# Performance work log

Measured on AMD Instinct MI355X. Metric: run time of the kernel, lower is better.

Reference implementation:

```python
import jax, jax.numpy as jnp
import numpy as np

N_NODES = 400
HID = 96
DEC = 64
FEAT_STATIC = 8
FEAT = FEAT_STATIC + N_NODES  # 408
EPS = 1e-8


def prelu(x, a):
    # single-parameter PReLU (torch default num_parameters=1)
    return jnp.where(x >= 0, x, a * x)


def setup_inputs() -> dict:
    key = jax.random.key(0)
    ks = jax.random.split(key, 16)
    B = 16
    E = N_NODES * (N_NODES - 1) // 2  # 79800

    x = jax.random.normal(ks[0], (B, E), dtype=jnp.float32)
    node_features = jax.random.normal(ks[1], (B, N_NODES, FEAT_STATIC), dtype=jnp.float32)
    sc_matrix = jax.random.uniform(ks[2], (B, N_NODES, N_NODES), dtype=jnp.float32)

    # normalization buffers (computed from train split in torch; random stand-ins)
    static_mean = jax.random.normal(ks[3], (1, 1, FEAT_STATIC), dtype=jnp.float32) * 0.1
    static_std = jnp.ones((1, 1, FEAT_STATIC), dtype=jnp.float32)

    def lin(k, fin, fout):
        kw, kb = jax.random.split(k)
        lim = 1.0 / np.sqrt(fin)
        W = jax.random.uniform(kw, (fin, fout), minval=-lim, maxval=lim, dtype=jnp.float32)
        b = jax.random.uniform(kb, (fout,), minval=-lim, maxval=lim, dtype=jnp.float32)
        return W, b

    W_e1, b_e1 = lin(ks[4], FEAT, HID)
    W_e2, b_e2 = lin(ks[5], HID, HID)
    W_d1, b_d1 = lin(ks[6], 3 * HID, DEC)  # symmetric decoder: 3 * node_embed_dim
    W_d2, b_d2 = lin(ks[7], DEC, DEC)
    W_d3, b_d3 = lin(ks[8], DEC, 1)

    a25 = jnp.float32(0.25)

    ei_np, ej_np = np.triu_indices(N_NODES, k=1)
    ei = jnp.asarray(ei_np, dtype=jnp.int32)
    ej = jnp.asarray(ej_np, dtype=jnp.int32)

    return {
        "x": x, "node_features": node_features, "sc_matrix": sc_matrix,
        "static_mean": static_mean, "static_std": static_std,
        "W_e1": W_e1, "b_e1": b_e1, "a_e1": a25,
        "W_e2": W_e2, "b_e2": b_e2, "a_e2": a25,
        "W_d1": W_d1, "b_d1": b_d1, "a_d1": a25,
        "W_d2": W_d2, "b_d2": b_d2, "a_d2": a25,
        "W_d3": W_d3, "b_d3": b_d3,
        "ei": ei, "ej": ej,
    }


def reference(x, node_features, sc_matrix, static_mean, static_std,
              W_e1, b_e1, a_e1, W_e2, b_e2, a_e2,
              W_d1, b_d1, a_d1, W_d2, b_d2, a_d2, W_d3, b_d3, ei, ej):
    # x (SC upper triangle) is only used for batch size in the torch module.
    # static anatomical block: z-score with train stats
    s = (node_features - static_mean) / (static_std + EPS)  # [B,N,8]
    # sc_row block, 'brain_scale': divide by per-matrix mean
    m = sc_matrix / jnp.maximum(
        jnp.mean(sc_matrix, axis=(-2, -1), keepdims=True), EPS)  # [B,N,N]
    feats = jnp.concatenate([s, m], axis=-1)  # [B,N,408]

    # shared node encoder (dropout inactive at eval)
    h = prelu(feats @ W_e1 + b_e1, a_e1)
    h = prelu(h @ W_e2 + b_e2, a_e2)  # [B,N,96]

    # per-edge gather over upper-triangle indices
    h_i = h[:, ei, :]  # [B,E,96]
    h_j = h[:, ej, :]
    # symmetric edge features
    edge_feat = jnp.concatenate(
        [h_i + h_j, jnp.abs(h_i - h_j), h_i * h_j], axis=-1)  # [B,E,288]

    z = prelu(edge_feat @ W_d1 + b_d1, a_d1)
    z = prelu(z @ W_d2 + b_d2, a_d2)
    out = (z @ W_d3 + b_d3)[..., 0]  # [B,E]
    return out
```

## Files before the change

kernel.cpp:

```cpp
#include <hip/hip_runtime.h>

#define NN 400
#define HID 96
#define EDGES 79800
#define BATCH 16
#define ROWS (BATCH*EDGES)
#define NT 13
#define NPAIRS 91

typedef _Float16 f16;
typedef f16 f16x2 __attribute__((ext_vector_type(2)));
typedef f16 f16x8 __attribute__((ext_vector_type(8)));
typedef __fp16 fp16x2 __attribute__((ext_vector_type(2)));
typedef float f32x16 __attribute__((ext_vector_type(16)));
typedef unsigned int u32;
typedef unsigned long long u64;

union H8 { f16x8 h; u32 u[4]; f16x2 p[4]; fp16x2 q[4]; u64 d[2]; };
union C2 { f16x2 h; fp16x2 q; u32 u; };

__device__ inline f16x2 pkrtz(float a, float b) {
  C2 c; c.q = __builtin_amdgcn_cvt_pkrtz(a, b); return c.h;
}
__device__ inline u32 pkrtz_u(float a, float b) {
  C2 c; c.q = __builtin_amdgcn_cvt_pkrtz(a, b); return c.u;
}
__device__ inline float fdot2a(f16x2 a, f16x2 b, float c) {
#if __has_builtin(__builtin_amdgcn_fdot2)
  C2 ca, cb; ca.h = a; cb.h = b;
  return __builtin_amdgcn_fdot2(ca.q, cb.q, c, false);
#else
  return c + (float)a.x*(float)b.x + (float)a.y*(float)b.y;
#endif
}

__device__ inline f16x8 habs8(f16x8 x) {
  H8 t; t.h = x;
  t.u[0] &= 0x7fff7fffu; t.u[1] &= 0x7fff7fffu;
  t.u[2] &= 0x7fff7fffu; t.u[3] &= 0x7fff7fffu;
  return t.h;
}

__device__ inline f16x8 pack8(float a0,float a1,float a2,float a3,
                              float a4,float a5,float a6,float a7){
  H8 u;
  u.p[0] = pkrtz(a0,a1);
  u.p[1] = pkrtz(a2,a3);
  u.p[2] = pkrtz(a4,a5);
  u.p[3] = pkrtz(a6,a7);
  return u.h;
}

__global__ void prep_mean_kernel(const float* __restrict__ We1, const float* __restrict__ We2,
                                 const float* __restrict__ W1, const float* __restrict__ W2,
                                 const float* __restrict__ sc,
                                 u32* __restrict__ wq, float* __restrict__ mpart) {
  if (blockIdx.x >= 140) {
    int p = blockIdx.x - 140;
    int b = p >> 4, part = p & 15;
    const float4* src = (const float4*)(sc + (size_t)b*160000) + part*2500;
    float s = 0.f;
    for (int i = threadIdx.x; i < 2500; i += 256) {
      float4 v = src[i];
      s += (v.x + v.y) + (v.z + v.w);
    }
    __shared__ float red[256];
    red[threadIdx.x] = s; __syncthreads();
    for (int off = 128; off > 0; off >>= 1) {
      if (threadIdx.x < off) red[threadIdx.x] += red[threadIdx.x + off];
      __syncthreads();
    }
    if (threadIdx.x == 0) mpart[p] = red[0];
    return;
  }
  int D = blockIdx.x*256 + threadIdx.x;
  float v0, v1;
  if (D < 9216) {
    int frag = D >> 8;  int t = frag >> 1, q = frag & 1;
    int rem = D & 255;  int lane = rem >> 2, dj = rem & 3;
    int c = lane & 31, h2 = lane >> 5;
    int k = 16*t + 8*h2 + 2*dj;
    int d = 32*q + c;
    v0 = W1[k*64 + d]; v1 = W1[(k+1)*64 + d];
  } else if (D < 11264) {
    int Dl = D - 9216;
    int frag = Dl >> 8; int t2 = frag >> 1, q = frag & 1;
    int rem = Dl & 255; int lane = rem >> 2, dj = rem & 3;
    int c = lane & 31, h2 = lane >> 5;
    int p = 8*t2 + 4*h2 + dj;
    int d = 32*q + c;
    v0 = W2[p*64 + d]; v1 = W2[(p+32)*64 + d];
  } else if (D < 31232) {
    int Dl = D - 11264;
    int frag = Dl >> 8; int t = frag/3, ct = frag - 3*t;
    int rem = Dl & 255; int lane = rem >> 2, dj = rem & 3;
    int c = lane & 31, h2 = lane >> 5;
    int k0 = 16*t + 8*h2 + 2*dj, k1 = k0 + 1;
    int d = 32*ct + c;
    v0 = (k0 < 400) ? We1[(8+k0)*96 + d] : (k0 < 408 ? We1[(k0-400)*96 + d] : 0.f);
    v1 = (k1 < 400) ? We1[(8+k1)*96 + d] : (k1 < 408 ? We1[(k1-400)*96 + d] : 0.f);
  } else {
    int Dl = D - 31232;
    int frag = Dl >> 8; int t = frag/3, ct = frag - 3*t;
    int rem = Dl & 255; int lane = rem >> 2, dj = rem & 3;
    int c = lane & 31, h2 = lane >> 5;
    int k = 16*t + 8*h2 + 2*dj;
    int d = 32*ct + c;
    v0 = We2[k*96 + d]; v1 = We2[(k+1)*96 + d];
  }
  wq[D] = pkrtz_u(v0, v1);
}

__global__ __launch_bounds__(256) void enc_kernel(
    const float* __restrict__ sc, const float* __restrict__ nf,
    const float* __restrict__ smean, const float* __restrict__ sstd,
    const float* __restrict__ be1, const float* __restrict__ ae1,
    const float* __restrict__ be2, const float* __restrict__ ae2,
    const float* __restrict__ mpart, const u32* __restrict__ wq,
    f16* __restrict__ hout) {
  __shared__ u32 lds[12288 + 1664];
  const int tid = threadIdx.x;
  const int wid = tid >> 6, lane = tid & 63;
  const int c = lane & 31, h2 = lane >> 5;
  const int r0 = blockIdx.x * 32;
  {
    int row = tid >> 3, seg = tid & 7;
    int r = r0 + row;
    int b = r / 400;
    float ms = 0.f;
    const float4* mp4 = (const float4*)(mpart + 16*b);
#pragma unroll
    for (int k = 0; k < 4; ++k) { float4 v = mp4[k]; ms += (v.x+v.y)+(v.z+v.w); }
    float rm = 1.f / fmaxf(ms*(1.f/160000.f), 1e-8f);
    const float4* src = (const float4*)(sc + (size_t)r*400);
#pragma unroll
    for (int i = 0; i < 13; ++i) {
      int col4 = seg + 8*i;
      if (col4 < 100) {
        float4 v = src[col4];
        u32 lo = pkrtz_u(v.x*rm, v.y*rm);
        u32 hi = pkrtz_u(v.z*rm, v.w*rm);
        *(u64*)(lds + row*210 + col4*2) = (u64)lo | ((u64)hi << 32);
      }
    }
  }
  __syncthreads();
  int tb = (wid==0) ? 0 : (wid==1) ? 7 : (wid==2) ? 14 : 20;
  int te = (wid==0) ? 7 : (wid==1) ? 14 : (wid==2) ? 20 : 26;
  f32x16 acc[3] = {};
  const u32* wb1 = wq + 11264;
  for (int t = tb; t < te; ++t) {
    f16x8 af;
    if (t < 25) {
      H8 av;
      const u32* ap = lds + c*210 + 8*t + 4*h2;
      av.d[0] = *(const u64*)ap;
      av.d[1] = *(const u64*)(ap + 2);
      af = av.h;
    } else {
      af = (f16x8){};
      if (h2 == 0) {
        int r = r0 + c;
        float q0[8];
#pragma unroll
        for (int j = 0; j < 8; ++j)
          q0[j] = (nf[r*8 + j] - smean[j]) / (sstd[j] + 1e-8f);
        af = pack8(q0[0],q0[1],q0[2],q0[3],q0[4],q0[5],q0[6],q0[7]);
      }
    }
#pragma unroll
    for (int ct = 0; ct < 3; ++ct) {
      f16x8 bf = *(const f16x8*)(wb1 + ((t*3+ct)*64 + lane)*4);
      acc[ct] = __builtin_amdgcn_mfma_f32_32x32x16_f16(af, bf, acc[ct], 0,0,0);
    }
  }
  __syncthreads();
#pragma unroll
  for (int ct = 0; ct < 3; ++ct) {
    union { f32x16 v; float4 f[4]; } u; u.v = acc[ct];
#pragma unroll
    for (int i4 = 0; i4 < 4; ++i4)
      *(float4*)(lds + (((wid*3+ct)*4 + i4)*64 + lane)*4) = u.f[i4];
  }
  __syncthreads();
  f16* zb16 = (f16*)(lds + 12288);
  const float a1 = *ae1;
  if (wid < 3) {
    float bv = be1[32*wid + c];
    f32x16 s;
#pragma unroll
    for (int i = 0; i < 16; ++i) s[i] = bv;
#pragma unroll
    for (int w2 = 0; w2 < 4; ++w2) {
#pragma unroll
      for (int i4 = 0; i4 < 4; ++i4) {
        float4 f = *(const float4*)(lds + (((w2*3+wid)*4 + i4)*64 + lane)*4);
        s[4*i4+0] += f.x; s[4*i4+1] += f.y; s[4*i4+2] += f.z; s[4*i4+3] += f.w;
      }
    }
#pragma unroll
    for (int r = 0; r < 16; ++r) {
      float v = s[r]; v = fmaxf(v, a1*v);
      int row = (r & 3) + 8*(r >> 2) + 4*h2;
      zb16[row*104 + 32*wid + c] = (f16)v;
    }
  }
  __syncthreads();
  if (wid < 3) {
    const float a2 = *ae2;
    float bv = be2[32*wid + c];
    f32x16 acc2;
#pragma unroll
    for (int i = 0; i < 16; ++i) acc2[i] = bv;
    const u32* wb2 = wq + 31232;
#pragma unroll
    for (int t = 0; t < 6; ++t) {
      f16x8 af = *(const f16x8*)(zb16 + c*104 + 16*t + 8*h2);
      f16x8 bf = *(const f16x8*)(wb2 + ((t*3+wid)*64 + lane)*4);
      acc2 = __builtin_amdgcn_mfma_f32_32x32x16_f16(af, bf, acc2, 0,0,0);
    }
#pragma unroll
    for (int rr = 0; rr < 16; ++rr) {
      int row = (rr & 3) + 8*(rr >> 2) + 4*h2;
      float v = acc2[rr]; v = fmaxf(v, a2*v);
      hout[(r0 + row)*96 + 32*wid + c] = (f16)v;
    }
  }
}

__global__ __launch_bounds__(256, 2) void decoder_kernel(
    const f16* __restrict__ hbuf, const u32* __restrict__ wq,
    const float* __restrict__ b1, const float* __restrict__ b2,
    const float* __restrict__ ad1, const float* __restrict__ ad2,
    const float* __restrict__ W3, const float* __restrict__ b3p,
    float* __restrict__ out) {
  __shared__ alignas(16) u32 smem[15360];
  const int tid = threadIdx.x;
  int p = blockIdx.x;
  int b = p / NPAIRS, pr = p - b*NPAIRS;
  int I = 0;
  while (pr >= NT - I) { pr -= NT - I; ++I; }
  const int J = I + pr;
  {
    for (int idx = tid; idx < 384; idx += 256) {
      int rr = idx / 12, ch = idx - rr*12;
      int nb = I*32 + rr;
      nb = nb < NN ? nb : NN-1;
      *(float4*)(smem + rr*48 + ch*4) =
          *(const float4*)(hbuf + (size_t)(b*NN + nb)*HID + ch*8);
    }
  }
  {
    float4* dst = (float4*)(smem + 1536);
    const float4* srcw = (const float4*)wq;
#pragma unroll
    for (int k = 0; k < 9; ++k) dst[tid + 256*k] = srcw[tid + 256*k];
  }

  const int lane = tid & 63;
  const int wid  = tid >> 6;
  const int c = lane & 31, h2 = lane >> 5;
  f16x8 hjr[6];
  {
    int nbJ = J*32 + c; nbJ = nbJ < NN ? nbJ : NN-1;
    const f16* hjrow = hbuf + (size_t)(b*NN + nbJ)*HID + 8*h2;
#pragma unroll
    for (int t = 0; t < 6; ++t) hjr[t] = *(const f16x8*)(hjrow + 16*t);
  }
  __syncthreads();

  const f16* hIlds = (const f16*)smem;
  const f16* wfr = (const f16*)(smem + 1536);
  u32* zb = smem + 10752 + wid*1152;
  f16x8 w2f[4][2];
#pragma unroll
  for (int t2 = 0; t2 < 4; ++t2) {
    w2f[t2][0] = *(const f16x8*)(wq + 9216 + ((t2*2+0)*64 + lane)*4);
    w2f[t2][1] = *(const f16x8*)(wq + 9216 + ((t2*2+1)*64 + lane)*4);
  }
  const float b1x = b1[c], b1y = b1[c+32];
  const float b2x = b2[c], b2y = b2[c+32];
  const float a1 = *ad1, a2 = *ad2, b3 = *b3p;
  const f16x2 a1v = pkrtz(a1, a1);
  const f16x2 a2v = pkrtz(a2, a2);
  const f16x2 w3p = pkrtz(W3[c], W3[c+32]);
  const f16x2 ones2 = pkrtz(1.f, 1.f);
  const int gj = J*32 + c;
  const int bofs = b*EDGES;

  for (int it = 0; it < 4; ++it) {
    const int i0 = it*8 + wid*2;
    const f16* hi0p = hIlds + (i0+0)*HID + 8*h2;
    const f16* hi1p = hIlds + (i0+1)*HID + 8*h2;
    f32x16 acc[2][2];
#pragma unroll
    for (int r = 0; r < 16; ++r) {
      acc[0][0][r] = b1x; acc[0][1][r] = b1y;
      acc[1][0][r] = b1x; acc[1][1][r] = b1y;
    }
#pragma unroll
    for (int t = 0; t < 6; ++t) {
      f16x8 bs0 = *(const f16x8*)(wfr + (((t   )*2+0)*64 + lane)*8);
      f16x8 bs1 = *(const f16x8*)(wfr + (((t   )*2+1)*64 + lane)*8);
      f16x8 bd0 = *(const f16x8*)(wfr + (((t+ 6)*2+0)*64 + lane)*8);
      f16x8 bd1 = *(const f16x8*)(wfr + (((t+ 6)*2+1)*64 + lane)*8);
      f16x8 bp0 = *(const f16x8*)(wfr + (((t+12)*2+0)*64 + lane)*8);
      f16x8 bp1 = *(const f16x8*)(wfr + (((t+12)*2+1)*64 + lane)*8);
      f16x8 hj = hjr[t];
#pragma unroll
      for (int m = 0; m < 2; ++m) {
        f16x8 hi = *(const f16x8*)((m ? hi1p : hi0p) + 16*t);
        f16x8 su = hi + hj;
        f16x8 di = habs8(hi - hj);
        f16x8 prd = hi * hj;
        acc[m][0] = __builtin_amdgcn_mfma_f32_32x32x16_f16(su, bs0, acc[m][0], 0,0,0);
        acc[m][1] = __builtin_amdgcn_mfma_f32_32x32x16_f16(su, bs1, acc[m][1], 0,0,0);
        acc[m][0] = __builtin_amdgcn_mfma_f32_32x32x16_f16(di, bd0, acc[m][0], 0,0,0);
        acc[m][1] = __builtin_amdgcn_mfma_f32_32x32x16_f16(di, bd1, acc[m][1], 0,0,0);
        acc[m][0] = __builtin_amdgcn_mfma_f32_32x32x16_f16(prd, bp0, acc[m][0], 0,0,0);
        acc[m][1] = __builtin_amdgcn_mfma_f32_32x32x16_f16(prd, bp1, acc[m][1], 0,0,0);
      }
    }
#pragma unroll
    for (int m = 0; m < 2; ++m) {
#pragma unroll
      for (int r = 0; r < 16; ++r) {
        f16x2 pz = pkrtz(acc[m][0][r], acc[m][1][r]);
        pz = __builtin_elementwise_max(pz, pz * a1v);
        C2 cv; cv.h = pz;
        int row = (r & 3) + 8*(r >> 2) + 4*h2;
        zb[row*36 + c] = cv.u;
      }
      f16x8 za[4];
#pragma unroll
      for (int t2 = 0; t2 < 4; ++t2)
        za[t2] = *(const f16x8*)((const f16*)zb + (c*36 + 8*t2 + 4*h2)*2);
      f32x16 zacc[2];
#pragma unroll
      for (int r = 0; r < 16; ++r) { zacc[0][r] = b2x; zacc[1][r] = b2y; }
#pragma unroll
      for (int t2 = 0; t2 < 4; ++t2) {
        zacc[0] = __builtin_amdgcn_mfma_f32_32x32x16_f16(za[t2], w2f[t2][0], zacc[0], 0,0,0);
        zacc[1] = __builtin_amdgcn_mfma_f32_32x32x16_f16(za[t2], w2f[t2][1], zacc[1], 0,0,0);
      }
#pragma unroll
      for (int r = 0; r < 16; ++r) {
        f16x2 pz = pkrtz(zacc[0][r], zacc[1][r]);
        pz = __builtin_elementwise_max(pz, pz * a2v);
        pz = pz * w3p;
        C2 cv; cv.h = pz;
        int row = (r & 3) + 8*(r >> 2) + 4*h2;
        zb[row*36 + c] = cv.u;
      }
      float ssum = 0.f;
#pragma unroll
      for (int g = 0; g < 4; ++g) {
        H8 v; v.h = *(const f16x8*)((const f16*)zb + (c*36 + 16*h2 + 4*g)*2);
#pragma unroll
        for (int dw = 0; dw < 4; ++dw)
          ssum = fdot2a(v.p[dw], ones2, ssum);
      }
      ssum += __shfl_xor(ssum, 32);
      int gi = I*32 + i0 + m;
      bool valid = (gi < gj) && (gj < NN);
      if (h2 == 0 && valid) {
        int eo = bofs + gi*(799 - gi)/2 + (gj - gi - 1);
        out[eo] = ssum + b3;
      }
    }
  }
}

extern "C" void kernel_launch(void* const* d_in, const int* in_sizes, int n_in,
                              void* d_out, int out_size, void* d_ws, size_t ws_size,
                              hipStream_t stream) {
  const float* nf  = (const float*)d_in[1];
  const float* sc  = (const float*)d_in[2];
  const float* sm  = (const float*)d_in[3];
  const float* ss  = (const float*)d_in[4];
  const float* We1 = (const float*)d_in[5];
  const float* be1 = (const float*)d_in[6];
  const float* ae1 = (const float*)d_in[7];
  const float* We2 = (const float*)d_in[8];
  const float* be2 = (const float*)d_in[9];
  const float* ae2 = (const float*)d_in[10];
  const float* W1  = (const float*)d_in[11];
  const float* b1  = (const float*)d_in[12];
  const float* a1  = (const float*)d_in[13];
  const float* W2  = (const float*)d_in[14];
  const float* b2  = (const float*)d_in[15];
  const float* a2  = (const float*)d_in[16];
  const float* W3  = (const float*)d_in[17];
  const float* b3  = (const float*)d_in[18];
  float* out = (float*)d_out;

  char* ws = (char*)d_ws;
  float* mpart = (float*)ws;
  f16*   hbuf = (f16*)(ws + 1024);
  u32*   wq   = (u32*)(ws + 1024 + 1228800);

  prep_mean_kernel<<<396, 256, 0, stream>>>(We1, We2, W1, W2, sc, wq, mpart);
  enc_kernel<<<200, 256, 0, stream>>>(sc, nf, sm, ss, be1, ae1, be2, ae2,
                                      mpart, wq, hbuf);
  decoder_kernel<<<BATCH*NPAIRS, 256, 0, stream>>>(hbuf, wq, b1, b2, a1, a2,
                                                   W3, b3, out);
}
```

Baseline: 185.6 us.

## Fuse prep, encoder and decoder into one persistent kernel with grid barriers

Replaces three kernel launches with a single persistent kernel of 512 blocks that runs weight packing and the mean reduction, the node encoder and then the edge decoder. Between phases it synchronises through atomic-counter grid barriers that are reset by a memset each call. The decoder now loops over pair tasks with a block stride and loads the decoder weights into shared memory once per block. The aim is to remove launch gaps and tail idling between stages. In exchange it adds barrier spin cost and an extra memset, and it relies on all 512 blocks being resident at once to avoid deadlock.

Measured after the change: 239.2 us. 1.29x slower.

```diff
diff --git a/kernel.cpp b/kernel.cpp
--- a/kernel.cpp
+++ b/kernel.cpp
@@ -7,6 +7,7 @@
 #define ROWS (BATCH*EDGES)
 #define NT 13
 #define NPAIRS 91
+#define NBLK 512
 
 typedef _Float16 f16;
 typedef f16 f16x2 __attribute__((ext_vector_type(2)));
@@ -51,321 +52,332 @@
   return u.h;
 }
 
-__global__ void prep_mean_kernel(const float* __restrict__ We1, const float* __restrict__ We2,
-                                 const float* __restrict__ W1, const float* __restrict__ W2,
-                                 const float* __restrict__ sc,
-                                 u32* __restrict__ wq, float* __restrict__ mpart) {
-  if (blockIdx.x >= 140) {
-    int p = blockIdx.x - 140;
+__device__ inline void grid_barrier(u32* ctr) {
+  __syncthreads();
+  if (threadIdx.x == 0) {
+    __builtin_amdgcn_fence(__ATOMIC_RELEASE, "agent");
+    atomicAdd(ctr, 1u);
+    while (__hip_atomic_load(ctr, __ATOMIC_RELAXED, __HIP_MEMORY_SCOPE_AGENT) < (u32)NBLK)
+      __builtin_amdgcn_s_sleep(2);
+    __builtin_amdgcn_fence(__ATOMIC_ACQUIRE, "agent");
+  }
+  __syncthreads();
+}
+
+__global__ __launch_bounds__(256, 2) void mega_kernel(
+    const float* __restrict__ nf, const float* __restrict__ sc,
+    const float* __restrict__ sm, const float* __restrict__ ss,
+    const float* __restrict__ We1, const float* __restrict__ be1, const float* __restrict__ ae1,
+    const float* __restrict__ We2, const float* __restrict__ be2, const float* __restrict__ ae2,
+    const float* __restrict__ W1, const float* __restrict__ b1, const float* __restrict__ ad1,
+    const float* __restrict__ W2, const float* __restrict__ b2, const float* __restrict__ ad2,
+    const float* __restrict__ W3, const float* __restrict__ b3p,
+    float* __restrict__ out, u32* __restrict__ ctr, float* __restrict__ mpart,
+    f16* __restrict__ hbuf, u32* __restrict__ wq)
+{
+  __shared__ alignas(16) u32 smem[15360];
+  const int tid = threadIdx.x;
+  const int bid = blockIdx.x;
+
+  if (bid < 140) {
+    int D = bid*256 + tid;
+    float v0, v1;
+    if (D < 9216) {
+      int frag = D >> 8;  int t = frag >> 1, q = frag & 1;
+      int rem = D & 255;  int lane = rem >> 2, dj = rem & 3;
+      int c = lane & 31, h2 = lane >> 5;
+      int k = 16*t + 8*h2 + 2*dj;
+      int d = 32*q + c;
+      v0 = W1[k*64 + d]; v1 = W1[(k+1)*64 + d];
+    } else if (D < 11264) {
+      int Dl = D - 9216;
+      int frag = Dl >> 8; int t2 = frag >> 1, q = frag & 1;
+      int rem = Dl & 255; int lane = rem >> 2, dj = rem & 3;
+      int c = lane & 31, h2 = lane >> 5;
+      int p = 8*t2 + 4*h2 + dj;
+      int d = 32*q + c;
+      v0 = W2[p*64 + d]; v1 = W2[(p+32)*64 + d];
+    } else if (D < 31232) {
+      int Dl = D - 11264;
+      int frag = Dl >> 8; int t = frag/3, ct = frag - 3*t;
+      int rem = Dl & 255; int lane = rem >> 2, dj = rem & 3;
+      int c = lane & 31, h2 = lane >> 5;
+      int k0 = 16*t + 8*h2 + 2*dj, k1 = k0 + 1;
+      int d = 32*ct + c;
+      v0 = (k0 < 400) ? We1[(8+k0)*96 + d] : (k0 < 408 ? We1[(k0-400)*96 + d] : 0.f);
+      v1 = (k1 < 400) ? We1[(8+k1)*96 + d] : (k1 < 408 ? We1[(k1-400)*96 + d] : 0.f);
+    } else {
+      int Dl = D - 31232;
+      int frag = Dl >> 8; int t = frag/3, ct = frag - 3*t;
+      int rem = Dl & 255; int lane = rem >> 2, dj = rem & 3;
+      int c = lane & 31, h2 = lane >> 5;
+      int k = 16*t + 8*h2 + 2*dj;
+      int d = 32*ct + c;
+      v0 = We2[k*96 + d]; v1 = We2[(k+1)*96 + d];
+    }
+    wq[D] = pkrtz_u(v0, v1);
+  } else if (bid < 396) {
+    int p = bid - 140;
     int b = p >> 4, part = p & 15;
     const float4* src = (const float4*)(sc + (size_t)b*160000) + part*2500;
     float s = 0.f;
-    for (int i = threadIdx.x; i < 2500; i += 256) {
+    for (int i = tid; i < 2500; i += 256) {
       float4 v = src[i];
       s += (v.x + v.y) + (v.z + v.w);
     }
-    __shared__ float red[256];
-    red[threadIdx.x] = s; __syncthreads();
+    float* red = (float*)smem;
+    red[tid] = s; __syncthreads();
     for (int off = 128; off > 0; off >>= 1) {
-      if (threadIdx.x < off) red[threadIdx.x] += red[threadIdx.x + off];
+      if (tid < off) red[tid] += red[tid + off];
       __syncthreads();
     }
-    if (threadIdx.x == 0) mpart[p] = red[0];
-    return;
+    if (tid == 0) mpart[p] = red[0];
   }
-  int D = blockIdx.x*256 + threadIdx.x;
-  float v0, v1;
-  if (D < 9216) {
-    int frag = D >> 8;  int t = frag >> 1, q = frag & 1;
-    int rem = D & 255;  int lane = rem >> 2, dj = rem & 3;
-    int c = lane & 31, h2 = lane >> 5;
-    int k = 16*t + 8*h2 + 2*dj;
-    int d = 32*q + c;
-    v0 = W1[k*64 + d]; v1 = W1[(k+1)*64 + d];
-  } else if (D < 11264) {
-    int Dl = D - 9216;
-    int frag = Dl >> 8; int t2 = frag >> 1, q = frag & 1;
-    int rem = Dl & 255; int lane = rem >> 2, dj = rem & 3;
-    int c = lane & 31, h2 = lane >> 5;
-    int p = 8*t2 + 4*h2 + dj;
-    int d = 32*q + c;
-    v0 = W2[p*64 + d]; v1 = W2[(p+32)*64 + d];
-  } else if (D < 31232) {
-    int Dl = D - 11264;
-    int frag = Dl >> 8; int t = frag/3, ct = frag - 3*t;
-    int rem = Dl & 255; int lane = rem >> 2, dj = rem & 3;
-    int c = lane & 31, h2 = lane >> 5;
-    int k0 = 16*t + 8*h2 + 2*dj, k1 = k0 + 1;
-    int d = 32*ct + c;
-    v0 = (k0 < 400) ? We1[(8+k0)*96 + d] : (k0 < 408 ? We1[(k0-400)*96 + d] : 0.f);
-    v1 = (k1 < 400) ? We1[(8+k1)*96 + d] : (k1 < 408 ? We1[(k1-400)*96 + d] : 0.f);
-  } else {
-    int Dl = D - 31232;
-    int frag = Dl >> 8; int t = frag/3, ct = frag - 3*t;
-    int rem = Dl & 255; int lane = rem >> 2, dj = rem & 3;
-    int c = lane & 31, h2 = lane >> 5;
-    int k = 16*t + 8*h2 + 2*dj;
-    int d = 32*ct + c;
-    v0 = We2[k*96 + d]; v1 = We2[(k+1)*96 + d];
+  grid_barrier(ctr);
+
+  if (bid < 200) {
+    u32* lds = smem;
+    const int wid = tid >> 6, lane = tid & 63;
+    const int c = lane & 31, h2 = lane >> 5;
+    const int r0 = bid * 32;
+    {
+      int row = tid >> 3, seg = tid & 7;
+      int r = r0 + row;
+      int b = r / 400;
+      float ms = 0.f;
+      const float4* mp4 = (const float4*)(mpart + 16*b);
+#pragma unroll
+      for (int k = 0; k < 4; ++k) { float4 v = mp4[k]; ms += (v.x+v.y)+(v.z+v.w); }
+      float rm = 1.f / fmaxf(ms*(1.f/160000.f), 1e-8f);
+      const float4* src = (const float4*)(sc + (size_t)r*400);
+#pragma unroll
+      for (int i = 0; i < 13; ++i) {
+        int col4 = seg + 8*i;
+        if (col4 < 100) {
+          float4 v = src[col4];
+          u32 lo = pkrtz_u(v.x*rm, v.y*rm);
+          u32 hi = pkrtz_u(v.z*rm, v.w*rm);
+          *(u64*)(lds + row*210 + col4*2) = (u64)lo | ((u64)hi << 32);
+        }
+      }
+    }
+    __syncthreads();
+    int tb = (wid==0) ? 0 : (wid==1) ? 7 : (wid==2) ? 14 : 20;
+    int te = (wid==0) ? 7 : (wid==1) ? 14 : (wid==2) ? 20 : 26;
+    f32x16 acc[3] = {};
+    const u32* wb1 = wq + 11264;
+    for (int t = tb; t < te; ++t) {
+      f16x8 af;
+      if (t < 25) {
+        H8 av;
+        const u32* ap = lds + c*210 + 8*t + 4*h2;
+        av.d[0] = *(const u64*)ap;
+        av.d[1] = *(const u64*)(ap + 2);
+        af = av.h;
+      } else {
+        af = (f16x8){};
+        if (h2 == 0) {
+          int r = r0 + c;
+          float q0[8];
+#pragma unroll
+          for (int j = 0; j < 8; ++j)
+            q0[j] = (nf[r*8 + j] - sm[j]) / (ss[j] + 1e-8f);
+          af = pack8(q0[0],q0[1],q0[2],q0[3],q0[4],q0[5],q0[6],q0[7]);
+        }
+      }
+#pragma unroll
+      for (int ct = 0; ct < 3; ++ct) {
+        f16x8 bf = *(const f16x8*)(wb1 + ((t*3+ct)*64 + lane)*4);
+        acc[ct] = __builtin_amdgcn_mfma_f32_32x32x16_f16(af, bf, acc[ct], 0,0,0);
+      }
+    }
+    __syncthreads();
+#pragma unroll
+    for (int ct = 0; ct < 3; ++ct) {
+      union { f32x16 v; float4 f[4]; } u; u.v = acc[ct];
+#pragma unroll
+      for (int i4 = 0; i4 < 4; ++i4)
+        *(float4*)(lds + (((wid*3+ct)*4 + i4)*64 + lane)*4) = u.f[i4];
+    }
+    __syncthreads();
+    f16* zb16 = (f16*)(lds + 12288);
+    const float a1 = *ae1;
+    if (wid < 3) {
+      float bv = be1[32*wid + c];
+      f32x16 s;
+#pragma unroll
+      for (int i = 0; i < 16; ++i) s[i] = bv;
+#pragma unroll
+      for (int w2 = 0; w2 < 4; ++w2) {
+#pragma unroll
+        for (int i4 = 0; i4 < 4; ++i4) {
+          float4 f = *(const float4*)(lds + (((w2*3+wid)*4 + i4)*64 + lane)*4);
+          s[4*i4+0] += f.x; s[4*i4+1] += f.y; s[4*i4+2] += f.z; s[4*i4+3] += f.w;
+        }
+      }
+#pragma unroll
+      for (int r = 0; r < 16; ++r) {
+        float v = s[r]; v = fmaxf(v, a1*v);
+        int row = (r & 3) + 8*(r >> 2) + 4*h2;
+        zb16[row*104 + 32*wid + c] = (f16)v;
+      }
+    }
+    __syncthreads();
+    if (wid < 3) {
+      const float a2 = *ae2;
+      float bv = be2[32*wid + c];
+      f32x16 acc2;
+#pragma unroll
+      for (int i = 0; i < 16; ++i) acc2[i] = bv;
+      const u32* wb2 = wq + 31232;
+#pragma unroll
+      for (int t = 0; t < 6; ++t) {
+        f16x8 af = *(const f16x8*)(zb16 + c*104 + 16*t + 8*h2);
+        f16x8 bf = *(const f16x8*)(wb2 + ((t*3+wid)*64 + lane)*4);
+        acc2 = __builtin_amdgcn_mfma_f32_32x32x16_f16(af, bf, acc2, 0,0,0);
+      }
+#pragma unroll
+      for (int rr = 0; rr < 16; ++rr) {
+        int row = (rr & 3) + 8*(rr >> 2) + 4*h2;
+        float v = acc2[rr]; v = fmaxf(v, a2*v);
+        hbuf[(r0 + row)*96 + 32*wid + c] = (f16)v;
+      }
+    }
   }
-  wq[D] = pkrtz_u(v0, v1);
-}
-
-__global__ __launch_bounds__(256) void enc_kernel(
-    const float* __restrict__ sc, const float* __restrict__ nf,
-    const float* __restrict__ smean, const float* __restrict__ sstd,
-    const float* __restrict__ be1, const float* __restrict__ ae1,
-    const float* __restrict__ be2, const float* __restrict__ ae2,
-    const float* __restrict__ mpart, const u32* __restrict__ wq,
-    f16* __restrict__ hout) {
-  __shared__ u32 lds[12288 + 1664];
-  const int tid = threadIdx.x;
-  const int wid = tid >> 6, lane = tid & 63;
-  const int c = lane & 31, h2 = lane >> 5;
-  const int r0 = blockIdx.x * 32;
+  grid_barrier(ctr + 32);
+
   {
-    int row = tid >> 3, seg = tid & 7;
-    int r = r0 + row;
-    int b = r / 400;
-    float ms = 0.f;
-    const float4* mp4 = (const float4*)(mpart + 16*b);
-#pragma unroll
-    for (int k = 0; k < 4; ++k) { float4 v = mp4[k]; ms += (v.x+v.y)+(v.z+v.w); }
-    float rm = 1.f / fmaxf(ms*(1.f/160000.f), 1e-8f);
-    const float4* src = (const float4*)(sc + (size_t)r*400);
-#pragma unroll
-    for (int i = 0; i < 13; ++i) {
-      int col4 = seg + 8*i;
-      if (col4 < 100) {
-        float4 v = src[col4];
-        u32 lo = pkrtz_u(v.x*rm, v.y*rm);
-        u32 hi = pkrtz_u(v.z*rm, v.w*rm);
-        *(u64*)(lds + row*210 + col4*2) = (u64)lo | ((u64)hi << 32);
-      }
-    }
-  }
-  __syncthreads();
-  int tb = (wid==0) ? 0 : (wid==1) ? 7 : (wid==2) ? 14 : 20;
-  int te = (wid==0) ? 7 : (wid==1) ? 14 : (wid==2) ? 20 : 26;
-  f32x16 acc[3] = {};
-  const u32* wb1 = wq + 11264;
-  for (int t = tb; t < te; ++t) {
-    f16x8 af;
-    if (t < 25) {
-      H8 av;
-      const u32* ap = lds + c*210 + 8*t + 4*h2;
-      av.d[0] = *(const u64*)ap;
-      av.d[1] = *(const u64*)(ap + 2);
-      af = av.h;
-    } else {
-      af = (f16x8){};
-      if (h2 == 0) {
-        int r = r0 + c;
-        float q0[8];
-#pragma unroll
-        for (int j = 0; j < 8; ++j)
-          q0[j] = (nf[r*8 + j] - smean[j]) / (sstd[j] + 1e-8f);
-        af = pack8(q0[0],q0[1],q0[2],q0[3],q0[4],q0[5],q0[6],q0[7]);
-      }
-    }
-#pragma unroll
-    for (int ct = 0; ct < 3; ++ct) {
-      f16x8 bf = *(const f16x8*)(wb1 + ((t*3+ct)*64 + lane)*4);
-      acc[ct] = __builtin_amdgcn_mfma_f32_32x32x16_f16(af, bf, acc[ct], 0,0,0);
-    }
-  }
-  __syncthreads();
-#pragma unroll
-  for (int ct = 0; ct < 3; ++ct) {
-    union { f32x16 v; float4 f[4]; } u; u.v = acc[ct];
-#pragma unroll
-    for (int i4 = 0; i4 < 4; ++i4)
-      *(float4*)(lds + (((wid*3+ct)*4 + i4)*64 + lane)*4) = u.f[i4];
-  }
-  __syncthreads();
-  f16* zb16 = (f16*)(lds + 12288);
-  const float a1 = *ae1;
-  if (wid < 3) {
-    float bv = be1[32*wid + c];
-    f32x16 s;
-#pragma unroll
-    for (int i = 0; i < 16; ++i) s[i] = bv;
-#pragma unroll
-    for (int w2 = 0; w2 < 4; ++w2) {
-#pragma unroll
-      for (int i4 = 0; i4 < 4; ++i4) {
-        float4 f = *(const float4*)(lds + (((w2*3+wid)*4 + i4)*64 + lane)*4);
-        s[4*i4+0] += f.x; s[4*i4+1] += f.y; s[4*i4+2] += f.z; s[4*i4+3] += f.w;
-      }
-    }
-#pragma unroll
-    for (int r = 0; r < 16; ++r) {
-      float v = s[r]; v = fmaxf(v, a1*v);
-      int row = (r & 3) + 8*(r >> 2) + 4*h2;
-      zb16[row*104 + 32*wid + c] = (f16)v;
-    }
-  }
-  __syncthreads();
-  if (wid < 3) {
-    const float a2 = *ae2;
-    float bv = be2[32*wid + c];
-    f32x16 acc2;
-#pragma unroll
-    for (int i = 0; i < 16; ++i) acc2[i] = bv;
-    const u32* wb2 = wq + 31232;
-#pragma unroll
-    for (int t = 0; t < 6; ++t) {
-      f16x8 af = *(const f16x8*)(zb16 + c*104 + 16*t + 8*h2);
-      f16x8 bf = *(const f16x8*)(wb2 + ((t*3+wid)*64 + lane)*4);
-      acc2 = __builtin_amdgcn_mfma_f32_32x32x16_f16(af, bf, acc2, 0,0,0);
-    }
-#pragma unroll
-    for (int rr = 0; rr < 16; ++rr) {
-      int row = (rr & 3) + 8*(rr >> 2) + 4*h2;
-      float v = acc2[rr]; v = fmaxf(v, a2*v);
-      hout[(r0 + row)*96 + 32*wid + c] = (f16)v;
-    }
-  }
-}
-
-__global__ __launch_bounds__(256, 2) void decoder_kernel(
-    const f16* __restrict__ hbuf, const u32* __restrict__ wq,
-    const float* __restrict__ b1, const float* __restrict__ b2,
-    const float* __restrict__ ad1, const float* __restrict__ ad2,
-    const float* __restrict__ W3, const float* __restrict__ b3p,
-    float* __restrict__ out) {
-  __shared__ alignas(16) u32 smem[15360];
-  const int tid = threadIdx.x;
-  int p = blockIdx.x;
-  int b = p / NPAIRS, pr = p - b*NPAIRS;
-  int I = 0;
-  while (pr >= NT - I) { pr -= NT - I; ++I; }
-  const int J = I + pr;
-  {
-    for (int idx = tid; idx < 384; idx += 256) {
-      int rr = idx / 12, ch = idx - rr*12;
-      int nb = I*32 + rr;
-      nb = nb < NN ? nb : NN-1;
-      *(float4*)(smem + rr*48 + ch*4) =
-          *(const float4*)(hbuf + (size_t)(b*NN + nb)*HID + ch*8);
-    }
-  }
-  {
-    float4* dst = (float4*)(smem + 1536);
-    const float4* srcw = (const float4*)wq;
-#pragma unroll
-    for (int k = 0; k < 9; ++k) dst[tid + 256*k] = srcw[tid + 256*k];
-  }
-
-  const int lane = tid & 63;
-  const int wid  = tid >> 6;
-  const int c = lane & 31, h2 = lane >> 5;
-  f16x8 hjr[6];
-  {
-    int nbJ = J*32 + c; nbJ = nbJ < NN ? nbJ : NN-1;
-    const f16* hjrow = hbuf + (size_t)(b*NN + nbJ)*HID + 8*h2;
-#pragma unroll
-    for (int t = 0; t < 6; ++t) hjr[t] = *(const f16x8*)(hjrow + 16*t);
-  }
-  __syncthreads();
-
-  const f16* hIlds = (const f16*)smem;
-  const f16* wfr = (const f16*)(smem + 1536);
-  u32* zb = smem + 10752 + wid*1152;
-  f16x8 w2f[4][2];
-#pragma unroll
-  for (int t2 = 0; t2 < 4; ++t2) {
-    w2f[t2][0] = *(const f16x8*)(wq + 9216 + ((t2*2+0)*64 + lane)*4);
-    w2f[t2][1] = *(const f16x8*)(wq + 9216 + ((t2*2+1)*64 + lane)*4);
-  }
-  const float b1x = b1[c], b1y = b1[c+32];
-  const float b2x = b2[c], b2y = b2[c+32];
-  const float a1 = *ad1, a2 = *ad2, b3 = *b3p;
-  const f16x2 a1v = pkrtz(a1, a1);
-  const f16x2 a2v = pkrtz(a2, a2);
-  const f16x2 w3p = pkrtz(W3[c], W3[c+32]);
-  const f16x2 ones2 = pkrtz(1.f, 1.f);
-  const int gj = J*32 + c;
-  const int bofs = b*EDGES;
-
-  for (int it = 0; it < 4; ++it) {
-    const int i0 = it*8 + wid*2;
-    const f16* hi0p = hIlds + (i0+0)*HID + 8*h2;
-    const f16* hi1p = hIlds + (i0+1)*HID + 8*h2;
-    f32x16 acc[2][2];
-#pragma unroll
-    for (int r = 0; r < 16; ++r) {
-      acc[0][0][r] = b1x; acc[0][1][r] = b1y;
-      acc[1][0][r] = b1x; acc[1][1][r] = b1y;
-    }
-#pragma unroll
-    for (int t = 0; t < 6; ++t) {
-      f16x8 bs0 = *(const f16x8*)(wfr + (((t   )*2+0)*64 + lane)*8);
-      f16x8 bs1 = *(const f16x8*)(wfr + (((t   )*2+1)*64 + lane)*8);
-      f16x8 bd0 = *(const f16x8*)(wfr + (((t+ 6)*2+0)*64 + lane)*8);
-      f16x8 bd1 = *(const f16x8*)(wfr + (((t+ 6)*2+1)*64 + lane)*8);
-      f16x8 bp0 = *(const f16x8*)(wfr + (((t+12)*2+0)*64 + lane)*8);
-      f16x8 bp1 = *(const f16x8*)(wfr + (((t+12)*2+1)*64 + lane)*8);
-      f16x8 hj = hjr[t];
-#pragma unroll
-      for (int m = 0; m < 2; ++m) {
-        f16x8 hi = *(const f16x8*)((m ? hi1p : hi0p) + 16*t);
-        f16x8 su = hi + hj;
-        f16x8 di = habs8(hi - hj);
-        f16x8 prd = hi * hj;
-        acc[m][0] = __builtin_amdgcn_mfma_f32_32x32x16_f16(su, bs0, acc[m][0], 0,0,0);
-        acc[m][1] = __builtin_amdgcn_mfma_f32_32x32x16_f16(su, bs1, acc[m][1], 0,0,0);
-        acc[m][0] = __builtin_amdgcn_mfma_f32_32x32x16_f16(di, bd0, acc[m][0], 0,0,0);
-        acc[m][1] = __builtin_amdgcn_mfma_f32_32x32x16_f16(di, bd1, acc[m][1], 0,0,0);
-        acc[m][0] = __builtin_amdgcn_mfma_f32_32x32x16_f16(prd, bp0, acc[m][0], 0,0,0);
-        acc[m][1] = __builtin_amdgcn_mfma_f32_32x32x16_f16(prd, bp1, acc[m][1], 0,0,0);
-      }
-    }
-#pragma unroll
-    for (int m = 0; m < 2; ++m) {
-#pragma unroll
-      for (int r = 0; r < 16; ++r) {
-        f16x2 pz = pkrtz(acc[m][0][r], acc[m][1][r]);
-        pz = __builtin_elementwise_max(pz, pz * a1v);
-        C2 cv; cv.h = pz;
-        int row = (r & 3) + 8*(r >> 2) + 4*h2;
-        zb[row*36 + c] = cv.u;
-      }
-      f16x8 za[4];
-#pragma unroll
-      for (int t2 = 0; t2 < 4; ++t2)
-        za[t2] = *(const f16x8*)((const f16*)zb + (c*36 + 8*t2 + 4*h2)*2);
-      f32x16 zacc[2];
-#pragma unroll
-      for (int r = 0; r < 16; ++r) { zacc[0][r] = b2x; zacc[1][r] = b2y; }
-#pragma unroll
-      for (int t2 = 0; t2 < 4; ++t2) {
-        zacc[0] = __builtin_amdgcn_mfma_f32_32x32x16_f16(za[t2], w2f[t2][0], zacc[0], 0,0,0);
-        zacc[1] = __builtin_amdgcn_mfma_f32_32x32x16_f16(za[t2], w2f[t2][1], zacc[1], 0,0,0);
-      }
-#pragma unroll
-      for (int r = 0; r < 16; ++r) {
-        f16x2 pz = pkrtz(zacc[0][r], zacc[1][r]);
-        pz = __builtin_elementwise_max(pz, pz * a2v);
-        pz = pz * w3p;
-        C2 cv; cv.h = pz;
-        int row = (r & 3) + 8*(r >> 2) + 4*h2;
-        zb[row*36 + c] = cv.u;
-      }
-      float ssum = 0.f;
-#pragma unroll
-      for (int g = 0; g < 4; ++g) {
-        H8 v; v.h = *(const f16x8*)((const f16*)zb + (c*36 + 16*h2 + 4*g)*2);
-#pragma unroll
-        for (int dw = 0; dw < 4; ++dw)
-          ssum = fdot2a(v.p[dw], ones2, ssum);
-      }
-      ssum += __shfl_xor(ssum, 32);
-      int gi = I*32 + i0 + m;
-      bool valid = (gi < gj) && (gj < NN);
-      if (h2 == 0 && valid) {
-        int eo = bofs + gi*(799 - gi)/2 + (gj - gi - 1);
-        out[eo] = ssum + b3;
+    const int lane = tid & 63;
+    const int wid  = tid >> 6;
+    const int c = lane & 31, h2 = lane >> 5;
+    __syncthreads();
+    {
+      float4* dst = (float4*)(smem + 1536);
+      const float4* srcw = (const float4*)wq;
+#pragma unroll
+      for (int k = 0; k < 9; ++k) dst[tid + 256*k] = srcw[tid + 256*k];
+    }
+    const f16* hIlds = (const f16*)smem;
+    const f16* wfr = (const f16*)(smem + 1536);
+    u32* zb = smem + 10752 + wid*1152;
+    f16x8 w2f[4][2];
+#pragma unroll
+    for (int t2 = 0; t2 < 4; ++t2) {
+      w2f[t2][0] = *(const f16x8*)(wq + 9216 + ((t2*2+0)*64 + lane)*4);
+      w2f[t2][1] = *(const f16x8*)(wq + 9216 + ((t2*2+1)*64 + lane)*4);
+    }
+    const float b1x = b1[c], b1y = b1[c+32];
+    const float b2x = b2[c], b2y = b2[c+32];
+    const float a1 = *ad1, a2 = *ad2, b3 = *b3p;
+    const f16x2 a1v = pkrtz(a1, a1);
+    const f16x2 a2v = pkrtz(a2, a2);
+    const f16x2 w3p = pkrtz(W3[c], W3[c+32]);
+    const f16x2 ones2 = pkrtz(1.f, 1.f);
+
+    for (int task = bid; task < BATCH*NPAIRS; task += NBLK) {
+      int b = task / NPAIRS, pr = task - b*NPAIRS;
+      int I = 0;
+      while (pr >= NT - I) { pr -= NT - I; ++I; }
+      const int J = I + pr;
+      __syncthreads();
+      for (int idx = tid; idx < 384; idx += 256) {
+        int rr = idx / 12, ch = idx - rr*12;
+        int nb = I*32 + rr;
+        nb = nb < NN ? nb : NN-1;
+        *(float4*)(smem + rr*48 + ch*4) =
+            *(const float4*)(hbuf + (size_t)(b*NN + nb)*HID + ch*8);
+      }
+      f16x8 hjr[6];
+      {
+        int nbJ = J*32 + c; nbJ = nbJ < NN ? nbJ : NN-1;
+        const f16* hjrow = hbuf + (size_t)(b*NN + nbJ)*HID + 8*h2;
+#pragma unroll
+        for (int t = 0; t < 6; ++t) hjr[t] = *(const f16x8*)(hjrow + 16*t);
+      }
+      __syncthreads();
+      const int gj = J*32 + c;
+      const int bofs = b*EDGES;
+
+      for (int it = 0; it < 4; ++it) {
+        const int i0 = it*8 + wid*2;
+        const f16* hi0p = hIlds + (i0+0)*HID + 8*h2;
+        const f16* hi1p = hIlds + (i0+1)*HID + 8*h2;
+        f32x16 acc[2][2];
+#pragma unroll
+        for (int r = 0; r < 16; ++r) {
+          acc[0][0][r] = b1x; acc[0][1][r] = b1y;
+          acc[1][0][r] = b1x; acc[1][1][r] = b1y;
+        }
+#pragma unroll
+        for (int t = 0; t < 6; ++t) {
+          f16x8 bs0 = *(const f16x8*)(wfr + (((t   )*2+0)*64 + lane)*8);
+          f16x8 bs1 = *(const f16x8*)(wfr + (((t   )*2+1)*64 + lane)*8);
+          f16x8 bd0 = *(const f16x8*)(wfr + (((t+ 6)*2+0)*64 + lane)*8);
+          f16x8 bd1 = *(const f16x8*)(wfr + (((t+ 6)*2+1)*64 + lane)*8);
+          f16x8 bp0 = *(const f16x8*)(wfr + (((t+12)*2+0)*64 + lane)*8);
+          f16x8 bp1 = *(const f16x8*)(wfr + (((t+12)*2+1)*64 + lane)*8);
+          f16x8 hj = hjr[t];
+#pragma unroll
+          for (int m = 0; m < 2; ++m) {
+            f16x8 hi = *(const f16x8*)((m ? hi1p : hi0p) + 16*t);
+            f16x8 su = hi + hj;
+            f16x8 di = habs8(hi - hj);
+            f16x8 prd = hi * hj;
+            acc[m][0] = __builtin_amdgcn_mfma_f32_32x32x16_f16(su, bs0, acc[m][0], 0,0,0);
+            acc[m][1] = __builtin_amdgcn_mfma_f32_32x32x16_f16(su, bs1, acc[m][1], 0,0,0);
+            acc[m][0] = __builtin_amdgcn_mfma_f32_32x32x16_f16(di, bd0, acc[m][0], 0,0,0);
+            acc[m][1] = __builtin_amdgcn_mfma_f32_32x32x16_f16(di, bd1, acc[m][1], 0,0,0);
+            acc[m][0] = __builtin_amdgcn_mfma_f32_32x32x16_f16(prd, bp0, acc[m][0], 0,0,0);
+            acc[m][1] = __builtin_amdgcn_mfma_f32_32x32x16_f16(prd, bp1, acc[m][1], 0,0,0);
+          }
+        }
+#pragma unroll
+        for (int m = 0; m < 2; ++m) {
+#pragma unroll
+          for (int r = 0; r < 16; ++r) {
+            f16x2 pz = pkrtz(acc[m][0][r], acc[m][1][r]);
+            pz = __builtin_elementwise_max(pz, pz * a1v);
+            C2 cv; cv.h = pz;
+            int row = (r & 3) + 8*(r >> 2) + 4*h2;
+            zb[row*36 + c] = cv.u;
+          }
+          f16x8 za[4];
+#pragma unroll
+          for (int t2 = 0; t2 < 4; ++t2)
+            za[t2] = *(const f16x8*)((const f16*)zb + (c*36 + 8*t2 + 4*h2)*2);
+          f32x16 zacc[2];
+#pragma unroll
+          for (int r = 0; r < 16; ++r) { zacc[0][r] = b2x; zacc[1][r] = b2y; }
+#pragma unroll
+          for (int t2 = 0; t2 < 4; ++t2) {
+            zacc[0] = __builtin_amdgcn_mfma_f32_32x32x16_f16(za[t2], w2f[t2][0], zacc[0], 0,0,0);
+            zacc[1] = __builtin_amdgcn_mfma_f32_32x32x16_f16(za[t2], w2f[t2][1], zacc[1], 0,0,0);
+          }
+#pragma unroll
+          for (int r = 0; r < 16; ++r) {
+            f16x2 pz = pkrtz(zacc[0][r], zacc[1][r]);
+            pz = __builtin_elementwise_max(pz, pz * a2v);
+            pz = pz * w3p;
+            C2 cv; cv.h = pz;
+            int row = (r & 3) + 8*(r >> 2) + 4*h2;
+            zb[row*36 + c] = cv.u;
+          }
+          float ssum = 0.f;
+#pragma unroll
+          for (int g = 0; g < 4; ++g) {
+            H8 v; v.h = *(const f16x8*)((const f16*)zb + (c*36 + 16*h2 + 4*g)*2);
+#pragma unroll
+            for (int dw = 0; dw < 4; ++dw)
+              ssum = fdot2a(v.p[dw], ones2, ssum);
+          }
+          ssum += __shfl_xor(ssum, 32);
+          int gi = I*32 + i0 + m;
+          bool valid = (gi < gj) && (gj < NN);
+          if (h2 == 0 && valid) {
+            int eo = bofs + gi*(799 - gi)/2 + (gj - gi - 1);
+            out[eo] = ssum + b3;
+          }
+        }
       }
     }
   }
@@ -395,13 +407,14 @@
   float* out = (float*)d_out;
 
   char* ws = (char*)d_ws;
-  float* mpart = (float*)ws;
-  f16*   hbuf = (f16*)(ws + 1024);
-  u32*   wq   = (u32*)(ws + 1024 + 1228800);
-
-  prep_mean_kernel<<<396, 256, 0, stream>>>(We1, We2, W1, W2, sc, wq, mpart);
-  enc_kernel<<<200, 256, 0, stream>>>(sc, nf, sm, ss, be1, ae1, be2, ae2,
-                                      mpart, wq, hbuf);
-  decoder_kernel<<<BATCH*NPAIRS, 256, 0, stream>>>(hbuf, wq, b1, b2, a1, a2,
-                                                   W3, b3, out);
-}
+  u32*   ctr   = (u32*)ws;
+  float* mpart = (float*)(ws + 256);
+  f16*   hbuf  = (f16*)(ws + 1280);
+  u32*   wq    = (u32*)(ws + 1280 + 1228800);
+
+  hipMemsetAsync(ctr, 0, 256, stream);
+  mega_kernel<<<NBLK, 256, 0, stream>>>(nf, sc, sm, ss, We1, be1, ae1,
+                                        We2, be2, ae2, W1, b1, a1,
+                                        W2, b2, a2, W3, b3,
+                                        out, ctr, mpart, hbuf, wq);
+}
```
